# Optimization experiments

Hardware: AMD Instinct MI355X
Metric: run time of the kernel (lower is better)

Reference implementation:

```python
import jax, jax.numpy as jnp
import numpy as np
from jax import lax

B, T, C, F = 64, 1152, 64, 8
L_DP, N_DP = 24, 12
NUM_CLASSES = 4


def setup_inputs() -> dict:
    key = jax.random.key(0)
    ks = jax.random.split(key, 8)
    num_chunks = T // L_DP
    return {
        "L_norm": jax.random.normal(ks[0], (B, C, C), jnp.float32) / C,
        "X_seq": jax.random.normal(ks[1], (B, T, C, F), jnp.float32),
        "deterministic": 1,
        "conv_kernel": jax.random.normal(ks[2], (32, 1, F, 8), jnp.float32) * 0.06,  # HWIO
        "ln_scale": jnp.ones((8,), jnp.float32),
        "ln_bias": jnp.zeros((8,), jnp.float32),
        "spatial_w": jax.random.normal(ks[3], (64, 4), jnp.float32) * 0.17,
        "W1": jax.random.normal(ks[4], (num_chunks * 64, 32), jnp.float32) * 0.02,
        "b1": jnp.zeros((32,), jnp.float32),
        "W2": jax.random.normal(ks[5], (32, NUM_CLASSES), jnp.float32) * 0.1,
        "b2": jnp.zeros((NUM_CLASSES,), jnp.float32),
    }


def _spike(x):
    return jnp.where(x > 0, 1.0, 0.0).astype(x.dtype)


def reference(L_norm, X_seq, deterministic, conv_kernel, ln_scale, ln_bias,
              spatial_w, W1, b1, W2, b2):
    # temporal conv over (T, C) spatial dims, F -> 8 channels, SAME padding
    ann = lax.conv_general_dilated(
        X_seq, conv_kernel, window_strides=(1, 1), padding="SAME",
        dimension_numbers=("NHWC", "HWIO", "NHWC"))
    # LayerNorm over last (feature) axis, eps=1e-6 (flax default)
    mu = jnp.mean(ann, axis=-1, keepdims=True)
    var = jnp.mean(jnp.square(ann - mu), axis=-1, keepdims=True)
    ann = (ann - mu) * lax.rsqrt(var + 1e-6) * ln_scale + ln_bias
    ann = jax.nn.relu(ann)
    # graph propagation + channel-spatial projection
    gx = jnp.einsum("bnm,btmf->btnf", L_norm, ann)          # (B,T,64,8)
    gx_csp = jnp.einsum("btcf,cs->btsf", gx, spatial_w)     # (B,T,4,8)
    snn_in = gx_csp.reshape(B, T, 32)

    # two-layer LIF recurrence over time (strictly sequential)
    def step(carry, x_t):
        mem1, mem2, mem_out = carry
        mem1 = mem1 * 0.8 + x_t
        spk1 = _spike(mem1 - 0.5)
        mem1 = mem1 - spk1 * 0.5
        mem2 = mem2 * 0.9 + spk1
        spk2 = _spike(mem2 - 0.5)
        mem2 = mem2 - spk2 * 0.5
        mem_out = mem_out * 0.95 + spk2
        return (mem1, mem2, mem_out), (mem_out, spk1, spk2)

    mem0 = jnp.zeros((B, 32), snn_in.dtype)
    _, (pot, spk1, spk2) = lax.scan(step, (mem0, mem0, mem0),
                                    jnp.swapaxes(snn_in, 0, 1))
    pot = jnp.swapaxes(pot, 0, 1)                           # (B,T,32)

    chunks = pot.reshape(B, T // L_DP, L_DP, 32)
    start_mean = jnp.mean(chunks[:, :, :N_DP, :], axis=2)
    end_mean = jnp.mean(chunks[:, :, -N_DP:, :], axis=2)
    flat = jnp.concatenate([start_mean, end_mean], axis=-1).reshape(B, -1)

    y = jax.nn.gelu(flat @ W1 + b1)   # flax nn.gelu default approximate=True
    logits = y @ W2 + b2
    firing_rate = (jnp.mean(spk1) + jnp.mean(spk2)) / 2.0
    return logits, firing_rate
```

## Files before the change

kernel.cpp:

```cpp
#include <hip/hip_runtime.h>
#include <hip/hip_fp16.h>
#include <math.h>

#define T_SEQ 1152

typedef _Float16 f16x8 __attribute__((ext_vector_type(8)));
typedef float f32x4 __attribute__((ext_vector_type(4)));

__global__ void mKernel(const float* __restrict__ L, const float* __restrict__ sw,
                        float* __restrict__ Mbuf) {
  int b = blockIdx.x, tid = threadIdx.x;
  int s = tid >> 6, m = tid & 63;
  float a = 0.f;
  #pragma unroll 4
  for (int n = 0; n < 64; ++n)
    a = fmaf(sw[n * 4 + s], L[(b * 64 + n) * 64 + m], a);
  Mbuf[b * 256 + m * 4 + s] = a;
}

__global__ __launch_bounds__(256, 4)
void convKernel(const float* __restrict__ X, const float* __restrict__ Kw,
                const float* __restrict__ lnS, const float* __restrict__ lnB,
                const float* __restrict__ Mbuf, float* __restrict__ snn) {
  __shared__ int4   XS[2][8 * 65];
  __shared__ float4 hT4[512];

  const int bid  = blockIdx.x;
  const int b    = bid / 36;
  const int tile = bid - b * 36;
  const int t0   = tile * 32;
  const int tid  = threadIdx.x;
  const int lane = tid & 63;
  const int wid  = tid >> 6;
  const int tcol = lane & 15;
  const int rg   = lane >> 4;
  const int fq   = rg & 1;
  const int tloc = tcol + ((rg >> 1) << 4);

  const int rA = lane & 15;
  const int fr = rA & 7;
  const int sh16 = (rA >> 3) << 4;
  f16x8 ka[12];
  #pragma unroll
  for (int q = 0; q < 12; ++q) {
    const int khs = 4 * q + rg - sh16;
    #pragma unroll
    for (int j = 0; j < 8; ++j) {
      float kv = (khs >= 0 && khs < 32) ? Kw[khs * 64 + j * 8 + fr] : 0.f;
      ka[q][j] = (_Float16)kv;
    }
  }

  const int tpt   = lane >> 1;
  const int cslot = lane & 1;

  const int sc2 = tid & 7;
  const int srow0 = tid >> 3;
  const int srow1 = srow0 + 32;
  const int st0 = t0 - 15 + srow0;
  const int st1 = t0 - 15 + srow1;
  const bool v0 = (st0 >= 0) && (st0 < T_SEQ);
  const bool v1 = (srow1 < 63) && (st1 >= 0) && (st1 < T_SEQ);
  const float* xb = X + (size_t)(b * T_SEQ) * 512;

  float pacc[4][8];
  #pragma unroll
  for (int s = 0; s < 4; ++s)
    #pragma unroll
    for (int f = 0; f < 8; ++f) pacc[s][f] = 0.f;

  const float4 z4 = make_float4(0.f, 0.f, 0.f, 0.f);

#define CVT_WRITE(BUF, P0, P1, Q0, Q1)                                       \
  { {                                                                        \
      unsigned u0 = __builtin_bit_cast(unsigned, __float22half2_rn(make_float2(P0.x, P0.y))); \
      unsigned u1 = __builtin_bit_cast(unsigned, __float22half2_rn(make_float2(P0.z, P0.w))); \
      unsigned u2 = __builtin_bit_cast(unsigned, __float22half2_rn(make_float2(P1.x, P1.y))); \
      unsigned u3 = __builtin_bit_cast(unsigned, __float22half2_rn(make_float2(P1.z, P1.w))); \
      int4 v; v.x = (int)u0; v.y = (int)u1; v.z = (int)u2; v.w = (int)u3;    \
      XS[BUF][sc2 * 65 + srow0] = v;                                         \
    }                                                                        \
    if (srow1 < 63) {                                                        \
      unsigned u0 = __builtin_bit_cast(unsigned, __float22half2_rn(make_float2(Q0.x, Q0.y))); \
      unsigned u1 = __builtin_bit_cast(unsigned, __float22half2_rn(make_float2(Q0.z, Q0.w))); \
      unsigned u2 = __builtin_bit_cast(unsigned, __float22half2_rn(make_float2(Q1.x, Q1.y))); \
      unsigned u3 = __builtin_bit_cast(unsigned, __float22half2_rn(make_float2(Q1.z, Q1.w))); \
      int4 v; v.x = (int)u0; v.y = (int)u1; v.z = (int)u2; v.w = (int)u3;    \
      XS[BUF][sc2 * 65 + srow1] = v;                                         \
    } }

  {
    const float* xp = xb + sc2 * 8;
    float4 a0 = z4, a1 = z4, b0 = z4, b1 = z4;
    if (v0) { const float* p = xp + (size_t)st0 * 512; a0 = *(const float4*)p; a1 = *(const float4*)(p + 4); }
    if (v1) { const float* p = xp + (size_t)st1 * 512; b0 = *(const float4*)p; b1 = *(const float4*)(p + 4); }
    CVT_WRITE(0, a0, a1, b0, b1)
  }
  __syncthreads();

  #pragma unroll 1
  for (int part = 0; part < 8; ++part) {
    float4 pa0 = z4, pa1 = z4, pb0 = z4, pb1 = z4;
    if (part < 7) {
      const float* xp = xb + ((part + 1) * 8 + sc2) * 8;
      if (v0) { const float* p = xp + (size_t)st0 * 512; pa0 = *(const float4*)p; pa1 = *(const float4*)(p + 4); }
      if (v1) { const float* p = xp + (size_t)st1 * 512; pb0 = *(const float4*)p; pb1 = *(const float4*)(p + 4); }
    }

    const int4* xsb = XS[part & 1];
    #pragma unroll
    for (int cp = 0; cp < 2; ++cp) {
      f32x4 acc = {0.f, 0.f, 0.f, 0.f};
      const int rb = (wid * 2 + cp) * 65 + tcol + rg;
      #pragma unroll
      for (int q = 0; q < 12; ++q) {
        f16x8 xf = __builtin_bit_cast(f16x8, xsb[rb + 4 * q]);
        acc = __builtin_amdgcn_mfma_f32_16x16x32_f16(ka[q], xf, acc, 0, 0, 0);
      }
      float4 st; st.x = acc[0]; st.y = acc[1]; st.z = acc[2]; st.w = acc[3];
      hT4[wid * 128 + cp * 64 + fq * 32 + tloc] = st;
    }

    {
      float4 lo = hT4[wid * 128 + cslot * 64 + tpt];
      float4 hi = hT4[wid * 128 + cslot * 64 + 32 + tpt];
      float hv[8] = { lo.x, lo.y, lo.z, lo.w, hi.x, hi.y, hi.z, hi.w };
      float mu = 0.f;
      #pragma unroll
      for (int f = 0; f < 8; ++f) mu += hv[f];
      mu *= 0.125f;
      float var = 0.f;
      #pragma unroll
      for (int f = 0; f < 8; ++f) { float d = hv[f] - mu; hv[f] = d; var = fmaf(d, d, var); }
      float rs = 1.0f / sqrtf(var * 0.125f + 1e-6f);
      const int c = part * 8 + wid * 2 + cslot;
      const float4 Mc = *(const float4*)(Mbuf + b * 256 + c * 4);
      #pragma unroll
      for (int f = 0; f < 8; ++f) {
        float hh = fmaxf(fmaf(hv[f] * rs, lnS[f], lnB[f]), 0.f);
        pacc[0][f] = fmaf(hh, Mc.x, pacc[0][f]);
        pacc[1][f] = fmaf(hh, Mc.y, pacc[1][f]);
        pacc[2][f] = fmaf(hh, Mc.z, pacc[2][f]);
        pacc[3][f] = fmaf(hh, Mc.w, pacc[3][f]);
      }
    }

    if (part < 7) {
      CVT_WRITE((part + 1) & 1, pa0, pa1, pb0, pb1)
    }
    __syncthreads();
  }
#undef CVT_WRITE

  #pragma unroll
  for (int s = 0; s < 4; ++s)
    #pragma unroll
    for (int f = 0; f < 8; ++f)
      pacc[s][f] += __shfl_xor(pacc[s][f], 1, 64);

  float* R = (float*)hT4;
  #pragma unroll
  for (int pass = 0; pass < 2; ++pass) {
    __syncthreads();
    if (wid > 0 && cslot == 0) {
      #pragma unroll
      for (int s2 = 0; s2 < 2; ++s2)
        #pragma unroll
        for (int f = 0; f < 8; ++f)
          R[((wid - 1) * 32 + tpt) * 16 + s2 * 8 + f] = pacc[pass * 2 + s2][f];
    }
    __syncthreads();
    if (wid == 0 && cslot == 0) {
      float* op = snn + ((size_t)b * T_SEQ + t0 + tpt) * 32;
      #pragma unroll
      for (int s2 = 0; s2 < 2; ++s2) {
        const int s = pass * 2 + s2;
        float v[8];
        #pragma unroll
        for (int f = 0; f < 8; ++f)
          v[f] = pacc[s][f]
               + R[(0 * 32 + tpt) * 16 + s2 * 8 + f]
               + R[(1 * 32 + tpt) * 16 + s2 * 8 + f]
               + R[(2 * 32 + tpt) * 16 + s2 * 8 + f];
        *(float4*)(op + s * 8)     = make_float4(v[0], v[1], v[2], v[3]);
        *(float4*)(op + s * 8 + 4) = make_float4(v[4], v[5], v[6], v[7]);
      }
    }
  }
}

__global__ __launch_bounds__(64, 1)
void scanKernel(const float* __restrict__ snn, float* __restrict__ flat,
                float* __restrict__ spkPart) {
  const int tid = threadIdx.x;
  const int j = tid & 31;
  const int b = blockIdx.x * 2 + (tid >> 5);
  const float* base = snn + (size_t)b * T_SEQ * 32 + j;

  float m1 = 0.f, m2 = 0.f, mo = 0.f, s1 = 0.f, s2 = 0.f;
  float cur[24], nxt[24];
  #pragma unroll
  for (int u = 0; u < 24; ++u) cur[u] = base[(size_t)u * 32];

  #pragma unroll 1
  for (int ch = 0; ch < 48; ++ch) {
    if (ch < 47) {
      #pragma unroll
      for (int u = 0; u < 24; ++u) nxt[u] = base[(size_t)((ch + 1) * 24 + u) * 32];
    }
    float aS = 0.f, aE = 0.f;
    #pragma unroll
    for (int u = 0; u < 24; ++u) {
      m1 = m1 * 0.8f + cur[u];
      float sp1 = (m1 > 0.5f) ? 1.f : 0.f;  m1 -= sp1 * 0.5f;
      m2 = m2 * 0.9f + sp1;
      float sp2 = (m2 > 0.5f) ? 1.f : 0.f;  m2 -= sp2 * 0.5f;
      mo = mo * 0.95f + sp2;
      s1 += sp1; s2 += sp2;
      if (u < 12) aS += mo; else aE += mo;
    }
    flat[b * 3072 + ch * 64 + j]      = aS / 12.0f;
    flat[b * 3072 + ch * 64 + 32 + j] = aE / 12.0f;
    if (ch < 47) {
      #pragma unroll
      for (int u = 0; u < 24; ++u) cur[u] = nxt[u];
    }
  }
  for (int off = 16; off > 0; off >>= 1) {
    s1 += __shfl_down(s1, off, 32);
    s2 += __shfl_down(s2, off, 32);
  }
  if (j == 0) { spkPart[b * 2] = s1; spkPart[b * 2 + 1] = s2; }
}

__global__ void mlpKernel(const float* __restrict__ flat, const float* __restrict__ W1,
                          const float* __restrict__ b1, const float* __restrict__ W2,
                          const float* __restrict__ b2, const float* __restrict__ spkPart,
                          float* __restrict__ out) {
  if (blockIdx.x == 64) {
    if (threadIdx.x == 0) {
      float s1 = 0.f, s2 = 0.f;
      for (int i = 0; i < 64; ++i) { s1 += spkPart[2*i]; s2 += spkPart[2*i+1]; }
      out[256] = (s1 + s2) * 0.5f / (64.0f * 1152.0f * 32.0f);
    }
    return;
  }
  const int b = blockIdx.x;
  const int tid = threadIdx.x;
  const int u = tid & 31, kc = tid >> 5;
  __shared__ float red[256];
  __shared__ float ys[32];
  float p = 0.f;
  const int kbeg = kc * 384, kend = kbeg + 384;
  #pragma unroll 4
  for (int k = kbeg; k < kend; ++k)
    p = fmaf(flat[b*3072 + k], W1[k*32 + u], p);
  red[tid] = p;
  __syncthreads();
  if (kc == 0) {
    float y = b1[u];
    #pragma unroll
    for (int q = 0; q < 8; ++q) y += red[q*32 + u];
    float y3 = y * y * y;
    float th = tanhf(0.7978845608028654f * (y + 0.044715f * y3));
    ys[u] = 0.5f * y * (1.0f + th);
  }
  __syncthreads();
  if (tid < 4) {
    float accv = b2[tid];
    #pragma unroll
    for (int q = 0; q < 32; ++q) accv = fmaf(ys[q], W2[q*4 + tid], accv);
    out[b*4 + tid] = accv;
  }
}

extern "C" void kernel_launch(void* const* d_in, const int* in_sizes, int n_in,
                              void* d_out, int out_size, void* d_ws, size_t ws_size,
                              hipStream_t stream) {
  const float* L   = (const float*)d_in[0];
  const float* X   = (const float*)d_in[1];
  const float* Kw  = (const float*)d_in[3];
  const float* lnS = (const float*)d_in[4];
  const float* lnB = (const float*)d_in[5];
  const float* sw  = (const float*)d_in[6];
  const float* W1  = (const float*)d_in[7];
  const float* b1  = (const float*)d_in[8];
  const float* W2  = (const float*)d_in[9];
  const float* b2  = (const float*)d_in[10];

  float* ws   = (float*)d_ws;
  float* Mbuf = ws;
  float* snn  = Mbuf + 16384;
  float* flat = snn + 2359296;
  float* spk  = flat + 196608;
  float* out  = (float*)d_out;

  mKernel<<<64, 256, 0, stream>>>(L, sw, Mbuf);
  convKernel<<<2304, 256, 0, stream>>>(X, Kw, lnS, lnB, Mbuf, snn);
  scanKernel<<<32, 64, 0, stream>>>(snn, flat, spk);
  mlpKernel<<<65, 256, 0, stream>>>(flat, W1, b1, W2, b2, spk, out);
}
```

Before: 148.3 us.

## Triple-buffer scan loads, count spikes via ballot, and swizzle conv block order

The scan kernel now keeps three register buffers of prefetched chunks in flight instead of two, so global load latency has more room to hide behind the serial LIF recurrence. Spike counts are gathered with wave ballot plus popcount into one per-block counter, which removes the float accumulators and the final shuffle reduction. The MLP kernel's final reduction is adjusted to match the new per-block layout. The conv kernel remaps block indices so consecutive blocks come from different batches, spreading memory traffic across channels. The cost is higher register pressure in the single-wave scan kernel.

```diff
diff --git a/kernel.cpp b/kernel.cpp
--- a/kernel.cpp
+++ b/kernel.cpp
@@ -25,7 +25,8 @@
   __shared__ int4   XS[2][8 * 65];
   __shared__ float4 hT4[512];
 
-  const int bid  = blockIdx.x;
+  const int bid0 = blockIdx.x;
+  const int bid  = (bid0 & 7) * 288 + (bid0 >> 3);
   const int b    = bid / 36;
   const int tile = bid - b * 36;
   const int t0   = tile * 32;
@@ -196,41 +197,58 @@
   const int j = tid & 31;
   const int b = blockIdx.x * 2 + (tid >> 5);
   const float* base = snn + (size_t)b * T_SEQ * 32 + j;
-
-  float m1 = 0.f, m2 = 0.f, mo = 0.f, s1 = 0.f, s2 = 0.f;
-  float cur[24], nxt[24];
-  #pragma unroll
-  for (int u = 0; u < 24; ++u) cur[u] = base[(size_t)u * 32];
-
+  float* fb = flat + b * 3072;
+
+  float m1 = 0.f, m2 = 0.f, mo = 0.f;
+  unsigned scnt1 = 0u, scnt2 = 0u;
+  float A[24], B[24], C[24];
+
+#define ISSUE(BUF, CH)                                                     \
+  { const float* p_ = base + (size_t)(CH) * 24 * 32;                       \
+    _Pragma("unroll")                                                      \
+    for (int u = 0; u < 24; ++u) BUF[u] = p_[(size_t)u * 32]; }
+
+#define COMPUTE(BUF, CH)                                                   \
+  { float aS = 0.f, aE = 0.f;                                              \
+    _Pragma("unroll")                                                      \
+    for (int u = 0; u < 24; ++u) {                                         \
+      m1 = fmaf(m1, 0.8f, BUF[u]);                                         \
+      bool c1 = m1 > 0.5f;                                                 \
+      unsigned long long bm1 = __ballot(c1);                               \
+      float sp1 = c1 ? 1.f : 0.f;                                          \
+      m1 = fmaf(sp1, -0.5f, m1);                                           \
+      scnt1 += (unsigned)__popcll(bm1);                                    \
+      m2 = fmaf(m2, 0.9f, sp1);                                            \
+      bool c2 = m2 > 0.5f;                                                 \
+      unsigned long long bm2 = __ballot(c2);                               \
+      float sp2 = c2 ? 1.f : 0.f;                                          \
+      m2 = fmaf(sp2, -0.5f, m2);                                           \
+      scnt2 += (unsigned)__popcll(bm2);                                    \
+      mo = fmaf(mo, 0.95f, sp2);                                           \
+      if (u < 12) aS += mo; else aE += mo;                                 \
+    }                                                                      \
+    fb[(CH) * 64 + j]      = aS / 12.0f;                                   \
+    fb[(CH) * 64 + 32 + j] = aE / 12.0f; }
+
+  ISSUE(A, 0)
+  ISSUE(B, 1)
   #pragma unroll 1
-  for (int ch = 0; ch < 48; ++ch) {
-    if (ch < 47) {
-      #pragma unroll
-      for (int u = 0; u < 24; ++u) nxt[u] = base[(size_t)((ch + 1) * 24 + u) * 32];
-    }
-    float aS = 0.f, aE = 0.f;
-    #pragma unroll
-    for (int u = 0; u < 24; ++u) {
-      m1 = m1 * 0.8f + cur[u];
-      float sp1 = (m1 > 0.5f) ? 1.f : 0.f;  m1 -= sp1 * 0.5f;
-      m2 = m2 * 0.9f + sp1;
-      float sp2 = (m2 > 0.5f) ? 1.f : 0.f;  m2 -= sp2 * 0.5f;
-      mo = mo * 0.95f + sp2;
-      s1 += sp1; s2 += sp2;
-      if (u < 12) aS += mo; else aE += mo;
-    }
-    flat[b * 3072 + ch * 64 + j]      = aS / 12.0f;
-    flat[b * 3072 + ch * 64 + 32 + j] = aE / 12.0f;
-    if (ch < 47) {
-      #pragma unroll
-      for (int u = 0; u < 24; ++u) cur[u] = nxt[u];
-    }
-  }
-  for (int off = 16; off > 0; off >>= 1) {
-    s1 += __shfl_down(s1, off, 32);
-    s2 += __shfl_down(s2, off, 32);
-  }
-  if (j == 0) { spkPart[b * 2] = s1; spkPart[b * 2 + 1] = s2; }
+  for (int k = 0; k < 16; ++k) {
+    const int c0 = 3 * k;
+    ISSUE(C, c0 + 2)
+    COMPUTE(A, c0)
+    if (k < 15) ISSUE(A, c0 + 3)
+    COMPUTE(B, c0 + 1)
+    if (k < 15) ISSUE(B, c0 + 4)
+    COMPUTE(C, c0 + 2)
+  }
+#undef ISSUE
+#undef COMPUTE
+
+  if (tid == 0) {
+    spkPart[blockIdx.x * 2]     = (float)scnt1;
+    spkPart[blockIdx.x * 2 + 1] = (float)scnt2;
+  }
 }
 
 __global__ void mlpKernel(const float* __restrict__ flat, const float* __restrict__ W1,
@@ -240,7 +258,7 @@
   if (blockIdx.x == 64) {
     if (threadIdx.x == 0) {
       float s1 = 0.f, s2 = 0.f;
-      for (int i = 0; i < 64; ++i) { s1 += spkPart[2*i]; s2 += spkPart[2*i+1]; }
+      for (int i = 0; i < 32; ++i) { s1 += spkPart[2*i]; s2 += spkPart[2*i+1]; }
       out[256] = (s1 + s2) * 0.5f / (64.0f * 1152.0f * 32.0f);
     }
     return;
```

After: 162.0 us. +9.2%, slower.

## Interleave two batch recurrences per scan thread and remap conv block order

Applied to the files above, without the earlier changes.

The scan kernel now has each thread run two independent batch LIF recurrences interleaved, with double-buffered chunk loads (A/B ping-pong) and fmaf forms. The grid is halved to 16 blocks. This is meant to hide the serial dependency latency and the global-load latency of the sequential recurrence through instruction-level parallelism. Separately, the conv kernel remaps block IDs with a stride of 288, likely to spread consecutive blocks across XCDs for cache locality. The cost is fewer parallel waves and more register pressure in the scan.

```diff
diff --git a/kernel.cpp b/kernel.cpp
--- a/kernel.cpp
+++ b/kernel.cpp
@@ -25,7 +25,8 @@
   __shared__ int4   XS[2][8 * 65];
   __shared__ float4 hT4[512];
 
-  const int bid  = blockIdx.x;
+  const int bid0 = blockIdx.x;
+  const int bid  = (bid0 & 7) * 288 + (bid0 >> 3);
   const int b    = bid / 36;
   const int tile = bid - b * 36;
   const int t0   = tile * 32;
@@ -194,43 +195,69 @@
                 float* __restrict__ spkPart) {
   const int tid = threadIdx.x;
   const int j = tid & 31;
-  const int b = blockIdx.x * 2 + (tid >> 5);
-  const float* base = snn + (size_t)b * T_SEQ * 32 + j;
-
-  float m1 = 0.f, m2 = 0.f, mo = 0.f, s1 = 0.f, s2 = 0.f;
-  float cur[24], nxt[24];
-  #pragma unroll
-  for (int u = 0; u < 24; ++u) cur[u] = base[(size_t)u * 32];
-
+  const int pr = blockIdx.x * 2 + (tid >> 5);
+  const int b0 = pr * 2, b1 = b0 + 1;
+  const float* base0 = snn + (size_t)b0 * T_SEQ * 32 + j;
+  const float* base1 = snn + (size_t)b1 * T_SEQ * 32 + j;
+  float* f0 = flat + b0 * 3072;
+  float* f1 = flat + b1 * 3072;
+
+  float m10 = 0.f, m20 = 0.f, mo0 = 0.f, s10 = 0.f, s20 = 0.f;
+  float m11 = 0.f, m21 = 0.f, mo1 = 0.f, s11 = 0.f, s21 = 0.f;
+  float A0[24], A1[24], B0[24], B1[24];
+
+#define ISSUE(P0, P1, CH)                                                  \
+  { const float* pa_ = base0 + (size_t)(CH) * 24 * 32;                     \
+    const float* pb_ = base1 + (size_t)(CH) * 24 * 32;                     \
+    _Pragma("unroll")                                                      \
+    for (int u = 0; u < 24; ++u) { P0[u] = pa_[(size_t)u * 32];            \
+                                   P1[u] = pb_[(size_t)u * 32]; } }
+
+#define COMPUTE(P0, P1, CH)                                                \
+  { float aS0 = 0.f, aE0 = 0.f, aS1 = 0.f, aE1 = 0.f;                      \
+    _Pragma("unroll")                                                      \
+    for (int u = 0; u < 24; ++u) {                                         \
+      m10 = fmaf(m10, 0.8f, P0[u]);                                        \
+      float sp1a = (m10 > 0.5f) ? 1.f : 0.f;  m10 = fmaf(sp1a, -0.5f, m10);\
+      m20 = fmaf(m20, 0.9f, sp1a);                                         \
+      float sp2a = (m20 > 0.5f) ? 1.f : 0.f;  m20 = fmaf(sp2a, -0.5f, m20);\
+      mo0 = fmaf(mo0, 0.95f, sp2a);                                        \
+      s10 += sp1a; s20 += sp2a;                                            \
+      m11 = fmaf(m11, 0.8f, P1[u]);                                        \
+      float sp1b = (m11 > 0.5f) ? 1.f : 0.f;  m11 = fmaf(sp1b, -0.5f, m11);\
+      m21 = fmaf(m21, 0.9f, sp1b);                                         \
+      float sp2b = (m21 > 0.5f) ? 1.f : 0.f;  m21 = fmaf(sp2b, -0.5f, m21);\
+      mo1 = fmaf(mo1, 0.95f, sp2b);                                        \
+      s11 += sp1b; s21 += sp2b;                                            \
+      if (u < 12) { aS0 += mo0; aS1 += mo1; } else { aE0 += mo0; aE1 += mo1; } \
+    }                                                                      \
+    f0[(CH) * 64 + j]      = aS0 / 12.0f;                                  \
+    f0[(CH) * 64 + 32 + j] = aE0 / 12.0f;                                  \
+    f1[(CH) * 64 + j]      = aS1 / 12.0f;                                  \
+    f1[(CH) * 64 + 32 + j] = aE1 / 12.0f; }
+
+  ISSUE(A0, A1, 0)
   #pragma unroll 1
-  for (int ch = 0; ch < 48; ++ch) {
-    if (ch < 47) {
-      #pragma unroll
-      for (int u = 0; u < 24; ++u) nxt[u] = base[(size_t)((ch + 1) * 24 + u) * 32];
-    }
-    float aS = 0.f, aE = 0.f;
-    #pragma unroll
-    for (int u = 0; u < 24; ++u) {
-      m1 = m1 * 0.8f + cur[u];
-      float sp1 = (m1 > 0.5f) ? 1.f : 0.f;  m1 -= sp1 * 0.5f;
-      m2 = m2 * 0.9f + sp1;
-      float sp2 = (m2 > 0.5f) ? 1.f : 0.f;  m2 -= sp2 * 0.5f;
-      mo = mo * 0.95f + sp2;
-      s1 += sp1; s2 += sp2;
-      if (u < 12) aS += mo; else aE += mo;
-    }
-    flat[b * 3072 + ch * 64 + j]      = aS / 12.0f;
-    flat[b * 3072 + ch * 64 + 32 + j] = aE / 12.0f;
-    if (ch < 47) {
-      #pragma unroll
-      for (int u = 0; u < 24; ++u) cur[u] = nxt[u];
-    }
-  }
+  for (int chp = 0; chp < 24; ++chp) {
+    const int ch = chp * 2;
+    ISSUE(B0, B1, ch + 1)
+    COMPUTE(A0, A1, ch)
+    if (chp < 23) ISSUE(A0, A1, ch + 2)
+    COMPUTE(B0, B1, ch + 1)
+  }
+#undef ISSUE
+#undef COMPUTE
+
   for (int off = 16; off > 0; off >>= 1) {
-    s1 += __shfl_down(s1, off, 32);
-    s2 += __shfl_down(s2, off, 32);
-  }
-  if (j == 0) { spkPart[b * 2] = s1; spkPart[b * 2 + 1] = s2; }
+    s10 += __shfl_down(s10, off, 32);
+    s20 += __shfl_down(s20, off, 32);
+    s11 += __shfl_down(s11, off, 32);
+    s21 += __shfl_down(s21, off, 32);
+  }
+  if (j == 0) {
+    spkPart[b0 * 2] = s10; spkPart[b0 * 2 + 1] = s20;
+    spkPart[b1 * 2] = s11; spkPart[b1 * 2 + 1] = s21;
+  }
 }
 
 __global__ void mlpKernel(const float* __restrict__ flat, const float* __restrict__ W1,
@@ -297,6 +324,6 @@
 
   mKernel<<<64, 256, 0, stream>>>(L, sw, Mbuf);
   convKernel<<<2304, 256, 0, stream>>>(X, Kw, lnS, lnB, Mbuf, snn);
-  scanKernel<<<32, 64, 0, stream>>>(snn, flat, spk);
+  scanKernel<<<16, 64, 0, stream>>>(snn, flat, spk);
   mlpKernel<<<65, 256, 0, stream>>>(flat, W1, b1, W2, b2, spk, out);
 }
```

Result: slower. 177.7 us (+19.9%).
